# Kernel tuning notes

Hardware: AMD Instinct MI355X
Metric: run time of the kernel (lower is better)

The kernel has to match this reference:

```python
import jax, jax.numpy as jnp
import numpy as np

BRANCH = 16   # children per internal node
DEPTH = 4     # levels 0..4, leaves at level 4
IN = 512
HID = 512

def _level_sizes():
    return [BRANCH ** d for d in range(DEPTH + 1)]

def setup_inputs() -> dict:
    key = jax.random.key(0)
    ks = jax.random.split(key, 9)
    N = sum(_level_sizes())  # 69905
    x = jax.random.normal(ks[0], (N, IN), dtype=jnp.float32)
    s = 1.0 / np.sqrt(IN + HID)  # torch nn.Linear default init bound
    def lin(kw, kb):
        w = jax.random.uniform(kw, (HID, IN + HID), jnp.float32, -s, s)
        b = jax.random.uniform(kb, (HID,), jnp.float32, -s, s)
        return w, b
    wi_w, wi_b = lin(ks[1], ks[2])
    wf_w, wf_b = lin(ks[3], ks[4])
    wo_w, wo_b = lin(ks[5], ks[6])
    wu_w, wu_b = lin(ks[7], ks[8])
    return {"x": x, "wi_w": wi_w, "wi_b": wi_b, "wf_w": wf_w, "wf_b": wf_b,
            "wo_w": wo_w, "wo_b": wo_b, "wu_w": wu_w, "wu_b": wu_b}

def reference(x, wi_w, wi_b, wf_w, wf_b, wo_w, wo_b, wu_w, wu_b):
    sizes = _level_sizes()
    offs = np.concatenate([[0], np.cumsum(sizes)])
    levels = [x[offs[d]:offs[d + 1]] for d in range(DEPTH + 1)]

    def gates(xh):
        i = jax.nn.sigmoid(xh @ wi_w.T + wi_b)
        o = jax.nn.sigmoid(xh @ wo_w.T + wo_b)
        u = jnp.tanh(xh @ wu_w.T + wu_b)
        return i, o, u

    # leaf_forward: h_prev = 0, no forget terms
    Xl = levels[DEPTH]
    xh = jnp.concatenate([Xl, jnp.zeros((Xl.shape[0], HID), Xl.dtype)], axis=1)
    i, o, u = gates(xh)
    C = i * u
    H = o * jnp.tanh(C)

    # node_forward, bottom-up. Faithful quirk of the source: the forget gate
    # is computed on the child CELL state (cat(x, c_k)), not the hidden state.
    for d in range(DEPTH - 1, -1, -1):
        Xd = levels[d]                      # [n, IN]
        n = Xd.shape[0]
        Hc = H.reshape(n, BRANCH, HID)      # children hidden
        Cc = C.reshape(n, BRANCH, HID)      # children cell
        h_sum = Hc.sum(axis=1)
        xh = jnp.concatenate([Xd, h_sum], axis=1)
        i, o, u = gates(xh)
        xc = jnp.concatenate([jnp.broadcast_to(Xd[:, None, :], (n, BRANCH, IN)), Cc], axis=-1)
        f = jax.nn.sigmoid(jnp.einsum('nbk,hk->nbh', xc, wf_w) + wf_b)
        C = i * u + (f * Cc).sum(axis=1)
        H = o * jnp.tanh(C)

    return H[0], C[0]
```

## Files before the change

kernel.cpp:

```cpp
#include <hip/hip_runtime.h>
#include <stdint.h>
#include <stddef.h>


typedef __bf16 bf16x8 __attribute__((ext_vector_type(8)));
typedef float  f32x4  __attribute__((ext_vector_type(4)));
typedef void __attribute__((address_space(3))) lds_void_t;
typedef void __attribute__((address_space(1))) gbl_void_t;

__device__ __forceinline__ uint16_t f2bf(float f) {
  union { float f; uint32_t u; } v; v.f = f;
  return (uint16_t)((v.u + 0x7fffu + ((v.u >> 16) & 1u)) >> 16);
}
__device__ __forceinline__ float bf2f(uint16_t u) {
  union { uint32_t u; float f; } v; v.u = (uint32_t)u << 16;
  return v.f;
}
__device__ __forceinline__ float sig_(float x) {
  return __builtin_amdgcn_rcpf(1.0f + __expf(-x));
}
__device__ __forceinline__ float tanh_(float x) {
  x = fminf(15.f, fmaxf(-15.f, x));
  float e = __expf(2.f * x);
  return (e - 1.f) * __builtin_amdgcn_rcpf(e + 1.f);
}

__global__ void k_conv_x(const float4* __restrict__ src,
                         ushort4* __restrict__ dst, long n4) {
  long i = blockIdx.x * (long)blockDim.x + threadIdx.x;
  long stride = (long)gridDim.x * blockDim.x;
  for (; i < n4; i += stride) {
    float4 v = src[i];
    ushort4 r;
    r.x = f2bf(v.x); r.y = f2bf(v.y); r.z = f2bf(v.z); r.w = f2bf(v.w);
    dst[i] = r;
  }
}
__global__ void k_conv_w(const float4* __restrict__ w0,
                         const float4* __restrict__ w1,
                         const float4* __restrict__ w2,
                         const float4* __restrict__ w3,
                         ushort4* __restrict__ dst) {
  const long per4 = (long)512 * 1024 / 4;
  long i = blockIdx.x * (long)blockDim.x + threadIdx.x;
  long stride = (long)gridDim.x * blockDim.x;
  for (; i < 4 * per4; i += stride) {
    long seg = i / per4, off2 = i - seg * per4;
    const float4* s = (seg == 0) ? w0 : (seg == 1) ? w1 : (seg == 2) ? w2 : w3;
    float4 v = s[off2];
    ushort4 r;
    r.x = f2bf(v.x); r.y = f2bf(v.y); r.z = f2bf(v.z); r.w = f2bf(v.w);
    dst[i] = r;
  }
}

#define BM 128
#define BN 128
#define BK 32

__global__ __launch_bounds__(256)
void k_gemm_bt(const uint16_t* __restrict__ A, int lda,
               const uint16_t* __restrict__ B, int ldb,
               float* __restrict__ C, int ldc, int K) {
  __shared__ uint16_t As[BM * BK];
  __shared__ uint16_t Bs[BN * BK];
  const int tid = threadIdx.x, lane = tid & 63, wave = tid >> 6;
  const int lrow = lane & 15, quad = lane >> 4;
  const int wm = (wave >> 1) * 64, wn = (wave & 1) * 64;
  const long tm = blockIdx.x, tn = blockIdx.y;
  f32x4 acc[4][4] = {};
  const int srow = lane >> 2, scol = (lane & 3) * 8;
  for (int k0 = 0; k0 < K; k0 += BK) {
#pragma unroll
    for (int i = 0; i < 2; ++i) {
      int row = i * 64 + wave * 16 + srow;
      const uint16_t* gp = A + (tm * BM + row) * (long)lda + k0 + scol;
      __builtin_amdgcn_global_load_lds((gbl_void_t*)(uintptr_t)gp,
          (lds_void_t*)&As[i * 2048 + wave * 512], 16, 0, 0);
    }
#pragma unroll
    for (int i = 0; i < 2; ++i) {
      int row = i * 64 + wave * 16 + srow;
      const uint16_t* gp = B + (tn * BN + row) * (long)ldb + k0 + scol;
      __builtin_amdgcn_global_load_lds((gbl_void_t*)(uintptr_t)gp,
          (lds_void_t*)&Bs[i * 2048 + wave * 512], 16, 0, 0);
    }
    __syncthreads();
    bf16x8 a[4], b[4];
#pragma unroll
    for (int f = 0; f < 4; ++f)
      a[f] = *(const bf16x8*)&As[(wm + f * 16 + lrow) * BK + quad * 8];
#pragma unroll
    for (int f = 0; f < 4; ++f)
      b[f] = *(const bf16x8*)&Bs[(wn + f * 16 + lrow) * BK + quad * 8];
#pragma unroll
    for (int fm = 0; fm < 4; ++fm)
#pragma unroll
      for (int fn = 0; fn < 4; ++fn)
        acc[fm][fn] = __builtin_amdgcn_mfma_f32_16x16x32_bf16(
            a[fm], b[fn], acc[fm][fn], 0, 0, 0);
    __syncthreads();
  }
#pragma unroll
  for (int fm = 0; fm < 4; ++fm)
#pragma unroll
    for (int fn = 0; fn < 4; ++fn) {
      long col  = tn * BN + wn + fn * 16 + lrow;
      long row0 = tm * BM + wm + fm * 16 + quad * 4;
#pragma unroll
      for (int r = 0; r < 4; ++r)
        C[(row0 + r) * (long)ldc + col] = acc[fm][fn][r];
    }
}

template <bool HAS_F>
__global__ __launch_bounds__(256, 3)
void k_level(const uint16_t* __restrict__ A, int lda, int K,
             const uint16_t* __restrict__ Wg,
             const float* __restrict__ bi, const float* __restrict__ bo,
             const float* __restrict__ bu,
             const float* __restrict__ Fpart,
             uint16_t* __restrict__ Cbf,
             const uint16_t* __restrict__ Xnext,
             uint16_t* __restrict__ xh_next) {
  __shared__ uint16_t As[2][128 * 32];
  __shared__ uint16_t Bs[2][3 * 64 * 32];
  const int tid = threadIdx.x, lane = tid & 63, wave = tid >> 6;
  const int lrow = lane & 15, quad = lane >> 4;
  const int wm = (wave >> 1) * 64, wn = (wave & 1) * 32;

  long tm, tn;
  {
    const int nTm = (int)(gridDim.x >> 3);
    int b = blockIdx.x;
    if ((nTm & 7) == 0) {
      int x = b & 7, j = b >> 3, per = nTm >> 3;
      tn = j & 7; tm = (long)x * per + (j >> 3);
    } else { tm = b >> 3; tn = b & 7; }
  }

  f32x4 acc[3][4][2] = {};
  const int srow = lane >> 2, scol = (lane & 3) * 8;

  for (int k0 = 0; k0 < K; k0 += 64) {
#pragma unroll
    for (int h = 0; h < 2; ++h) {
      int kk = k0 + h * 32;
#pragma unroll
      for (int i = 0; i < 2; ++i) {
        int row = i * 64 + wave * 16 + srow;
        const uint16_t* gp = A + (tm * 128 + row) * (long)lda + kk + scol;
        __builtin_amdgcn_global_load_lds((gbl_void_t*)(uintptr_t)gp,
            (lds_void_t*)&As[h][i * 2048 + wave * 512], 16, 0, 0);
      }
#pragma unroll
      for (int g = 0; g < 3; ++g) {
        long grow = g * 512 + tn * 64 + wave * 16 + srow;
        const uint16_t* gp = Wg + grow * 1024 + kk + scol;
        __builtin_amdgcn_global_load_lds((gbl_void_t*)(uintptr_t)gp,
            (lds_void_t*)&Bs[h][g * 2048 + wave * 512], 16, 0, 0);
      }
    }
    __syncthreads();

#pragma unroll
    for (int h = 0; h < 2; ++h) {
      bf16x8 a[4];
#pragma unroll
      for (int f = 0; f < 4; ++f)
        a[f] = *(const bf16x8*)&As[h][(wm + f * 16 + lrow) * 32 + quad * 8];
#pragma unroll
      for (int g = 0; g < 3; ++g) {
        bf16x8 b0 = *(const bf16x8*)&Bs[h][g * 2048 + (wn + lrow) * 32 +
                                           quad * 8];
        bf16x8 b1 = *(const bf16x8*)&Bs[h][g * 2048 + (wn + 16 + lrow) * 32 +
                                           quad * 8];
#pragma unroll
        for (int fm = 0; fm < 4; ++fm) {
          acc[g][fm][0] = __builtin_amdgcn_mfma_f32_16x16x32_bf16(
              a[fm], b0, acc[g][fm][0], 0, 0, 0);
          acc[g][fm][1] = __builtin_amdgcn_mfma_f32_16x16x32_bf16(
              a[fm], b1, acc[g][fm][1], 0, 0, 0);
        }
      }
    }
    __syncthreads();
  }

#pragma unroll
  for (int fn = 0; fn < 2; ++fn) {
    long col = tn * 64 + wn + fn * 16 + lrow;
    float biv = bi[col], bov = bo[col], buv = bu[col];
#pragma unroll
    for (int fm = 0; fm < 4; ++fm) {
      long row0 = tm * 128 + wm + fm * 16 + quad * 4;
      long pg   = tm * 8 + (wm >> 4) + fm;
      float hs = 0.f;
#pragma unroll
      for (int r = 0; r < 4; ++r) {
        long row = row0 + r;
        float iv = sig_(acc[0][fm][fn][r] + biv);
        float ov = sig_(acc[1][fm][fn][r] + bov);
        float uv = tanh_(acc[2][fm][fn][r] + buv);
        float c  = iv * uv;
        if (HAS_F) c += Fpart[row * 512 + col];
        Cbf[row * 512 + col] = f2bf(c);
        hs += ov * tanh_(c);
      }
      hs += __shfl_xor(hs, 16, 64);
      hs += __shfl_xor(hs, 32, 64);
      if (quad == 0) {
        xh_next[pg * 1024 + col]       = Xnext[pg * 512 + col];
        xh_next[pg * 1024 + 512 + col] = f2bf(hs);
      }
    }
  }
}

__global__ __launch_bounds__(256, 3)
void k_fc_combine(const uint16_t* __restrict__ Cbf,
                  const uint16_t* __restrict__ Wfc, int ldb,
                  const float* __restrict__ Fx,
                  const float* __restrict__ bfb,
                  float* __restrict__ Fpart) {
  __shared__ uint16_t As[2][BM * BK];
  __shared__ uint16_t Bs[2][BN * BK];
  const int tid = threadIdx.x, lane = tid & 63, wave = tid >> 6;
  const int lrow = lane & 15, quad = lane >> 4;
  const int wm = (wave >> 1) * 64, wn = (wave & 1) * 64;
  long tm, tn;
  {
    const int nTm = (int)(gridDim.x >> 2);
    int b = blockIdx.x;
    if ((nTm & 7) == 0) {
      int x = b & 7, j = b >> 3, per = nTm >> 3;
      tn = j & 3; tm = (long)x * per + (j >> 2);
    } else { tm = b >> 2; tn = b & 3; }
  }
  const int lda = 512;
  f32x4 acc[4][4] = {};
  const int srow = lane >> 2, scol = (lane & 3) * 8;
  for (int k0 = 0; k0 < 512; k0 += 64) {
#pragma unroll
    for (int h = 0; h < 2; ++h) {
      int kk = k0 + h * 32;
#pragma unroll
      for (int i = 0; i < 2; ++i) {
        int row = i * 64 + wave * 16 + srow;
        const uint16_t* gp = Cbf + (tm * BM + row) * (long)lda + kk + scol;
        __builtin_amdgcn_global_load_lds((gbl_void_t*)(uintptr_t)gp,
            (lds_void_t*)&As[h][i * 2048 + wave * 512], 16, 0, 0);
      }
#pragma unroll
      for (int i = 0; i < 2; ++i) {
        int row = i * 64 + wave * 16 + srow;
        const uint16_t* gp = Wfc + (tn * BN + row) * (long)ldb + kk + scol;
        __builtin_amdgcn_global_load_lds((gbl_void_t*)(uintptr_t)gp,
            (lds_void_t*)&Bs[h][i * 2048 + wave * 512], 16, 0, 0);
      }
    }
    __syncthreads();
#pragma unroll
    for (int h = 0; h < 2; ++h) {
      bf16x8 a[4], b[4];
#pragma unroll
      for (int f = 0; f < 4; ++f)
        a[f] = *(const bf16x8*)&As[h][(wm + f * 16 + lrow) * BK + quad * 8];
#pragma unroll
      for (int f = 0; f < 4; ++f)
        b[f] = *(const bf16x8*)&Bs[h][(wn + f * 16 + lrow) * BK + quad * 8];
#pragma unroll
      for (int fm = 0; fm < 4; ++fm)
#pragma unroll
        for (int fn = 0; fn < 4; ++fn)
          acc[fm][fn] = __builtin_amdgcn_mfma_f32_16x16x32_bf16(
              a[fm], b[fn], acc[fm][fn], 0, 0, 0);
    }
    __syncthreads();
  }
#pragma unroll
  for (int fm = 0; fm < 4; ++fm) {
    long pg   = tm * 8 + (wm >> 4) + fm;
    long row0 = tm * BM + wm + fm * 16 + quad * 4;
#pragma unroll
    for (int fn = 0; fn < 4; ++fn) {
      long col = tn * BN + wn + fn * 16 + lrow;
      float fx = Fx[pg * 512 + col] + bfb[col];
      float t = 0.f;
#pragma unroll
      for (int r = 0; r < 4; ++r)
        t += sig_(fx + acc[fm][fn][r]) * bf2f(Cbf[(row0 + r) * 512 + col]);
      t += __shfl_xor(t, 16, 64);
      t += __shfl_xor(t, 32, 64);
      if (quad == 0) Fpart[pg * 512 + col] = t;
    }
  }
}

__global__ void k_dot_bb(const uint16_t* __restrict__ A, int lda,
                         const uint16_t* __restrict__ B, int ldb,
                         float* __restrict__ C, int ldc,
                         int M, int N, int K) {
  int wid  = (int)((blockIdx.x * (long)blockDim.x + threadIdx.x) >> 6);
  int lane = threadIdx.x & 63;
  if (wid >= M * N) return;
  int m = wid / N, n = wid - m * N;
  const uint16_t* a = A + (long)m * lda;
  const uint16_t* b = B + (long)n * ldb;
  int per = K >> 6, k0 = lane * per;
  float s = 0.f;
  for (int j = 0; j < per; j += 4) {
    ushort4 av = *(const ushort4*)(a + k0 + j);
    ushort4 bv = *(const ushort4*)(b + k0 + j);
    s += bf2f(av.x) * bf2f(bv.x) + bf2f(av.y) * bf2f(bv.y)
       + bf2f(av.z) * bf2f(bv.z) + bf2f(av.w) * bf2f(bv.w);
  }
#pragma unroll
  for (int off = 32; off; off >>= 1) s += __shfl_xor(s, off, 64);
  if (lane == 0) C[(long)m * ldc + n] = s;
}
__global__ void k_dot_f32(const float* __restrict__ A, int lda,
                          const float* __restrict__ B, int ldb,
                          float* __restrict__ C, int ldc,
                          int M, int N, int K) {
  int wid  = (int)((blockIdx.x * (long)blockDim.x + threadIdx.x) >> 6);
  int lane = threadIdx.x & 63;
  if (wid >= M * N) return;
  int m = wid / N, n = wid - m * N;
  const float* a = A + (long)m * lda;
  const float* b = B + (long)n * ldb;
  int per = K >> 6, k0 = lane * per;
  float s = 0.f;
  for (int j = 0; j < per; j += 4) {
    float4 av = *(const float4*)(a + k0 + j);
    float4 bv = *(const float4*)(b + k0 + j);
    s += av.x * bv.x + av.y * bv.y + av.z * bv.z + av.w * bv.w;
  }
#pragma unroll
  for (int off = 32; off; off >>= 1) s += __shfl_xor(s, off, 64);
  if (lane == 0) C[(long)m * ldc + n] = s;
}

__global__ void k_hsum_xh4(const float* __restrict__ Hc,
                           const uint16_t* __restrict__ xd,
                           uint16_t* __restrict__ xh, int n) {
  long idx = blockIdx.x * (long)blockDim.x + threadIdx.x;
  if (idx >= (long)n * 128) return;
  long p = idx >> 7; int hq = (int)(idx & 127) << 2;
  const float* hp = Hc + (p << 4) * 512 + hq;
  float4 s = {0.f, 0.f, 0.f, 0.f};
#pragma unroll
  for (int b = 0; b < 16; ++b) {
    float4 v = *(const float4*)(hp + b * 512);
    s.x += v.x; s.y += v.y; s.z += v.z; s.w += v.w;
  }
  *(ushort4*)(xh + p * 1024 + hq) = *(const ushort4*)(xd + p * 512 + hq);
  ushort4 hw = {f2bf(s.x), f2bf(s.y), f2bf(s.z), f2bf(s.w)};
  *(ushort4*)(xh + p * 1024 + 512 + hq) = hw;
}

__global__ void k_combine4(const float* __restrict__ Fc,
                           const float* __restrict__ Fx,
                           const float* __restrict__ bfb,
                           const float* __restrict__ Cc,
                           float* __restrict__ Fpart, int nParents) {
  long idx = blockIdx.x * (long)blockDim.x + threadIdx.x;
  if (idx >= (long)nParents * 128) return;
  long pl = idx >> 7; int hq = (int)(idx & 127) << 2;
  float4 fxv = *(const float4*)(Fx + pl * 512 + hq);
  float4 bfv = *(const float4*)(bfb + hq);
  float fx0 = fxv.x + bfv.x, fx1 = fxv.y + bfv.y;
  float fx2 = fxv.z + bfv.z, fx3 = fxv.w + bfv.w;
  float a0 = 0.f, a1 = 0.f, a2 = 0.f, a3 = 0.f;
#pragma unroll 4
  for (int b = 0; b < 16; ++b) {
    long cl = pl * 16 + b;
    float4 f = *(const float4*)(Fc + cl * 512 + hq);
    float4 c = *(const float4*)(Cc + cl * 512 + hq);
    a0 += sig_(fx0 + f.x) * c.x;
    a1 += sig_(fx1 + f.y) * c.y;
    a2 += sig_(fx2 + f.z) * c.z;
    a3 += sig_(fx3 + f.w) * c.w;
  }
  float4 r = {a0, a1, a2, a3};
  *(float4*)(Fpart + pl * 512 + hq) = r;
}

__global__ void k_final4(const float* __restrict__ G,
                         const float* __restrict__ Fpart,
                         const float* __restrict__ bi,
                         const float* __restrict__ bo,
                         const float* __restrict__ bu,
                         float* __restrict__ H, float* __restrict__ Cv,
                         uint16_t* __restrict__ Cbf, int n) {
  long idx = blockIdx.x * (long)blockDim.x + threadIdx.x;
  if (idx >= (long)n * 128) return;
  long p = idx >> 7; int hq = (int)(idx & 127) << 2;
  const float* g = G + p * 1536;
  float4 gi = *(const float4*)(g + hq);
  float4 go = *(const float4*)(g + 512 + hq);
  float4 gu = *(const float4*)(g + 1024 + hq);
  float4 b_i = *(const float4*)(bi + hq);
  float4 b_o = *(const float4*)(bo + hq);
  float4 b_u = *(const float4*)(bu + hq);
  float4 fp = *(const float4*)(Fpart + p * 512 + hq);
  const float* gip = &gi.x; const float* gop = &go.x; const float* gup = &gu.x;
  const float* bip = &b_i.x; const float* bop = &b_o.x; const float* bup = &b_u.x;
  const float* fpp = &fp.x;
  float4 hv, cv;
  float* hvp = &hv.x; float* cvp = &cv.x;
  ushort4 cw; unsigned short* cwp = &cw.x;
#pragma unroll
  for (int j = 0; j < 4; ++j) {
    float iv = sig_(gip[j] + bip[j]);
    float ov = sig_(gop[j] + bop[j]);
    float uv = tanh_(gup[j] + bup[j]);
    float c  = iv * uv + fpp[j];
    cvp[j] = c;
    cwp[j] = f2bf(c);
    hvp[j] = ov * tanh_(c);
  }
  *(float4*)(H  + p * 512 + hq) = hv;
  *(float4*)(Cv + p * 512 + hq) = cv;
  *(ushort4*)(Cbf + p * 512 + hq) = cw;
}

extern "C" void kernel_launch(void* const* d_in, const int* in_sizes, int n_in,
                              void* d_out, int out_size, void* d_ws, size_t ws_size,
                              hipStream_t stream) {
  const float* x    = (const float*)d_in[0];
  const float* wi_w = (const float*)d_in[1];
  const float* wi_b = (const float*)d_in[2];
  const float* wf_w = (const float*)d_in[3];
  const float* wf_b = (const float*)d_in[4];
  const float* wo_w = (const float*)d_in[5];
  const float* wo_b = (const float*)d_in[6];
  const float* wu_w = (const float*)d_in[7];
  const float* wu_b = (const float*)d_in[8];
  (void)in_sizes; (void)n_in; (void)out_size; (void)ws_size;

  static const long offs[5] = {0, 1, 17, 273, 4369};
  const long NTOT = 69905;

  char* ws = (char*)d_ws;
  size_t off = 0;
  auto alloc = [&](size_t bytes) -> void* {
    void* p = ws + off;
    off += (bytes + 255) & ~(size_t)255;
    return p;
  };
  uint16_t* Xbf   = (uint16_t*)alloc(NTOT * 512 * 2);
  uint16_t* Wgw   = (uint16_t*)alloc((size_t)2048 * 1024 * 2);
  uint16_t* Wg    = Wgw;
  uint16_t* Wf    = Wgw + (size_t)1536 * 1024;
  float*    FxAll = (float*)alloc((size_t)4480 * 512 * 4);
  uint16_t* Cbf   = (uint16_t*)alloc((size_t)65536 * 512 * 2);
  uint16_t* CbfU  = (uint16_t*)alloc((size_t)4096 * 512 * 2);
  uint16_t* CbfU2 = (uint16_t*)alloc((size_t)256 * 512 * 2);
  uint16_t* xhA   = (uint16_t*)alloc((size_t)4096 * 1024 * 2);
  uint16_t* xhB   = (uint16_t*)alloc((size_t)256 * 1024 * 2);
  uint16_t* xhC   = (uint16_t*)alloc((size_t)16 * 1024 * 2);
  float*    Fpart = (float*)alloc((size_t)4096 * 512 * 4);
  float*    Gf    = (float*)alloc((size_t)16 * 1536 * 4);
  float*    Fc    = (float*)alloc((size_t)16 * 512 * 4);
  float*    HupA  = (float*)alloc((size_t)16 * 512 * 4);
  float*    CupA  = (float*)alloc((size_t)16 * 512 * 4);

  auto blks = [](long n) { return (int)((n + 255) / 256); };

  {
    long n4 = NTOT * 512 / 4;
    k_conv_x<<<8192, 256, 0, stream>>>((const float4*)x, (ushort4*)Xbf, n4);
    k_conv_w<<<2048, 256, 0, stream>>>((const float4*)wi_w, (const float4*)wo_w,
                                       (const float4*)wu_w, (const float4*)wf_w,
                                       (ushort4*)Wgw);
  }

  {
    dim3 grid(35, 4);
    k_gemm_bt<<<grid, 256, 0, stream>>>(Xbf, 512, Wf, 1024, FxAll, 512, 512);
  }

  k_level<false><<<4096, 256, 0, stream>>>(
      Xbf + offs[4] * 512, 512, 512, Wg, wi_b, wo_b, wu_b, nullptr,
      Cbf, Xbf + offs[3] * 512, xhA);
  k_fc_combine<<<2048, 256, 0, stream>>>(Cbf, Wf + 512, 1024,
                                         FxAll + offs[3] * 512, wf_b, Fpart);

  k_level<true><<<256, 256, 0, stream>>>(
      xhA, 1024, 1024, Wg, wi_b, wo_b, wu_b, Fpart,
      CbfU, Xbf + offs[2] * 512, xhB);
  k_fc_combine<<<128, 256, 0, stream>>>(CbfU, Wf + 512, 1024,
                                        FxAll + offs[2] * 512, wf_b, Fpart);

  k_level<true><<<16, 256, 0, stream>>>(
      xhB, 1024, 1024, Wg, wi_b, wo_b, wu_b, Fpart,
      CbfU2, Xbf + offs[1] * 512, xhC);
  k_fc_combine<<<8, 256, 0, stream>>>(CbfU2, Wf + 512, 1024,
                                      FxAll + offs[1] * 512, wf_b, Fpart);

  {
    long waves = 16L * 1536;
    k_dot_bb<<<(int)((waves * 64 + 255) / 256), 256, 0, stream>>>(
        xhC, 1024, Wg, 1024, Gf, 1536, 16, 1536, 1024);
    k_final4<<<blks(16L * 128), 256, 0, stream>>>(
        Gf, Fpart, wi_b, wo_b, wu_b, HupA, CupA, CbfU2, 16);
  }

  k_hsum_xh4<<<1, 256, 0, stream>>>(HupA, Xbf + offs[0] * 512, xhC, 1);
  {
    long waves = 1536;
    k_dot_bb<<<(int)((waves * 64 + 255) / 256), 256, 0, stream>>>(
        xhC, 1024, Wg, 1024, Gf, 1536, 1, 1536, 1024);
  }
  {
    long waves = 16L * 512;
    k_dot_f32<<<(int)((waves * 64 + 255) / 256), 256, 0, stream>>>(
        CupA, 512, wf_w + 512, 1024, Fc, 512, 16, 512, 512);
  }
  k_combine4<<<1, 256, 0, stream>>>(Fc, FxAll, wf_b, CupA, Fpart, 1);
  k_final4<<<1, 256, 0, stream>>>(
      Gf, Fpart, wi_b, wo_b, wu_b,
      (float*)d_out, (float*)d_out + 512, CbfU2, 1);
}
```

Measured before the change: 526.4 us.

## Double-buffer LDS tiles in level and fc GEMMs to overlap loads with MFMA

Both GEMM kernels now keep two LDS buffers and issue the global-to-LDS loads for the next K tile before computing the current one. Each stage ends with an explicit vmcnt wait and barrier, and MFMA sections run at raised wave priority. This is meant to hide global load latency that the old load-sync-compute-sync loop exposed. The doubled LDS footprint lowers the occupancy target from 3 to 2 blocks per CU. The change also switches f2bf to the native bf16 conversion and rewrites tanh as 2*sigmoid(2x)-1 to cut ALU work in the epilogues.

```diff
diff --git a/kernel.cpp b/kernel.cpp
--- a/kernel.cpp
+++ b/kernel.cpp
@@ -9,8 +9,9 @@
 typedef void __attribute__((address_space(1))) gbl_void_t;
 
 __device__ __forceinline__ uint16_t f2bf(float f) {
-  union { float f; uint32_t u; } v; v.f = f;
-  return (uint16_t)((v.u + 0x7fffu + ((v.u >> 16) & 1u)) >> 16);
+  union { __bf16 b; uint16_t u; } v;
+  v.b = (__bf16)f;
+  return v.u;
 }
 __device__ __forceinline__ float bf2f(uint16_t u) {
   union { uint32_t u; float f; } v; v.u = (uint32_t)u << 16;
@@ -20,9 +21,8 @@
   return __builtin_amdgcn_rcpf(1.0f + __expf(-x));
 }
 __device__ __forceinline__ float tanh_(float x) {
-  x = fminf(15.f, fmaxf(-15.f, x));
-  float e = __expf(2.f * x);
-  return (e - 1.f) * __builtin_amdgcn_rcpf(e + 1.f);
+  return __builtin_fmaf(2.f,
+      __builtin_amdgcn_rcpf(1.f + __expf(-2.f * x)), -1.f);
 }
 
 __global__ void k_conv_x(const float4* __restrict__ src,
@@ -114,7 +114,7 @@
 }
 
 template <bool HAS_F>
-__global__ __launch_bounds__(256, 3)
+__global__ __launch_bounds__(256, 2)
 void k_level(const uint16_t* __restrict__ A, int lda, int K,
              const uint16_t* __restrict__ Wg,
              const float* __restrict__ bi, const float* __restrict__ bo,
@@ -123,8 +123,8 @@
              uint16_t* __restrict__ Cbf,
              const uint16_t* __restrict__ Xnext,
              uint16_t* __restrict__ xh_next) {
-  __shared__ uint16_t As[2][128 * 32];
-  __shared__ uint16_t Bs[2][3 * 64 * 32];
+  __shared__ uint16_t As[2][2][128 * 32];
+  __shared__ uint16_t Bs[2][2][3 * 64 * 32];
   const int tid = threadIdx.x, lane = tid & 63, wave = tid >> 6;
   const int lrow = lane & 15, quad = lane >> 4;
   const int wm = (wave >> 1) * 64, wn = (wave & 1) * 32;
@@ -142,39 +142,42 @@
   f32x4 acc[3][4][2] = {};
   const int srow = lane >> 2, scol = (lane & 3) * 8;
 
-  for (int k0 = 0; k0 < K; k0 += 64) {
+  auto stage = [&](int kt, int buf) {
 #pragma unroll
     for (int h = 0; h < 2; ++h) {
-      int kk = k0 + h * 32;
+      int kk = kt * 64 + h * 32;
 #pragma unroll
       for (int i = 0; i < 2; ++i) {
         int row = i * 64 + wave * 16 + srow;
         const uint16_t* gp = A + (tm * 128 + row) * (long)lda + kk + scol;
         __builtin_amdgcn_global_load_lds((gbl_void_t*)(uintptr_t)gp,
-            (lds_void_t*)&As[h][i * 2048 + wave * 512], 16, 0, 0);
+            (lds_void_t*)&As[buf][h][i * 2048 + wave * 512], 16, 0, 0);
       }
 #pragma unroll
       for (int g = 0; g < 3; ++g) {
         long grow = g * 512 + tn * 64 + wave * 16 + srow;
         const uint16_t* gp = Wg + grow * 1024 + kk + scol;
         __builtin_amdgcn_global_load_lds((gbl_void_t*)(uintptr_t)gp,
-            (lds_void_t*)&Bs[h][g * 2048 + wave * 512], 16, 0, 0);
-      }
-    }
-    __syncthreads();
-
+            (lds_void_t*)&Bs[buf][h][g * 2048 + wave * 512], 16, 0, 0);
+      }
+    }
+  };
+
+  auto compute = [&](int buf) {
 #pragma unroll
     for (int h = 0; h < 2; ++h) {
       bf16x8 a[4];
 #pragma unroll
       for (int f = 0; f < 4; ++f)
-        a[f] = *(const bf16x8*)&As[h][(wm + f * 16 + lrow) * 32 + quad * 8];
+        a[f] = *(const bf16x8*)&As[buf][h][(wm + f * 16 + lrow) * 32 +
+                                           quad * 8];
 #pragma unroll
       for (int g = 0; g < 3; ++g) {
-        bf16x8 b0 = *(const bf16x8*)&Bs[h][g * 2048 + (wn + lrow) * 32 +
-                                           quad * 8];
-        bf16x8 b1 = *(const bf16x8*)&Bs[h][g * 2048 + (wn + 16 + lrow) * 32 +
-                                           quad * 8];
+        bf16x8 b0 = *(const bf16x8*)&Bs[buf][h][g * 2048 + (wn + lrow) * 32 +
+                                                quad * 8];
+        bf16x8 b1 = *(const bf16x8*)&Bs[buf][h][g * 2048 +
+                                                (wn + 16 + lrow) * 32 +
+                                                quad * 8];
 #pragma unroll
         for (int fm = 0; fm < 4; ++fm) {
           acc[g][fm][0] = __builtin_amdgcn_mfma_f32_16x16x32_bf16(
@@ -184,7 +187,25 @@
         }
       }
     }
-    __syncthreads();
+  };
+
+  const int NT = K >> 6;
+  stage(0, 0);
+  asm volatile("s_waitcnt vmcnt(0)" ::: "memory");
+  __builtin_amdgcn_s_barrier();
+  for (int kt = 0; kt < NT; kt += 2) {
+    stage(kt + 1, 1);
+    __builtin_amdgcn_s_setprio(1);
+    compute(0);
+    __builtin_amdgcn_s_setprio(0);
+    asm volatile("s_waitcnt vmcnt(0)" ::: "memory");
+    __builtin_amdgcn_s_barrier();
+    if (kt + 2 < NT) stage(kt + 2, 0);
+    __builtin_amdgcn_s_setprio(1);
+    compute(1);
+    __builtin_amdgcn_s_setprio(0);
+    asm volatile("s_waitcnt vmcnt(0)" ::: "memory");
+    __builtin_amdgcn_s_barrier();
   }
 
 #pragma unroll
@@ -217,14 +238,14 @@
   }
 }
 
-__global__ __launch_bounds__(256, 3)
+__global__ __launch_bounds__(256, 2)
 void k_fc_combine(const uint16_t* __restrict__ Cbf,
                   const uint16_t* __restrict__ Wfc, int ldb,
                   const float* __restrict__ Fx,
                   const float* __restrict__ bfb,
                   float* __restrict__ Fpart) {
-  __shared__ uint16_t As[2][BM * BK];
-  __shared__ uint16_t Bs[2][BN * BK];
+  __shared__ uint16_t As[2][2][BM * BK];
+  __shared__ uint16_t Bs[2][2][BN * BK];
   const int tid = threadIdx.x, lane = tid & 63, wave = tid >> 6;
   const int lrow = lane & 15, quad = lane >> 4;
   const int wm = (wave >> 1) * 64, wn = (wave & 1) * 64;
@@ -240,35 +261,40 @@
   const int lda = 512;
   f32x4 acc[4][4] = {};
   const int srow = lane >> 2, scol = (lane & 3) * 8;
-  for (int k0 = 0; k0 < 512; k0 += 64) {
+
+  auto stage = [&](int kt, int buf) {
 #pragma unroll
     for (int h = 0; h < 2; ++h) {
-      int kk = k0 + h * 32;
+      int kk = kt * 64 + h * 32;
 #pragma unroll
       for (int i = 0; i < 2; ++i) {
         int row = i * 64 + wave * 16 + srow;
         const uint16_t* gp = Cbf + (tm * BM + row) * (long)lda + kk + scol;
         __builtin_amdgcn_global_load_lds((gbl_void_t*)(uintptr_t)gp,
-            (lds_void_t*)&As[h][i * 2048 + wave * 512], 16, 0, 0);
+            (lds_void_t*)&As[buf][h][i * 2048 + wave * 512], 16, 0, 0);
       }
 #pragma unroll
       for (int i = 0; i < 2; ++i) {
         int row = i * 64 + wave * 16 + srow;
         const uint16_t* gp = Wfc + (tn * BN + row) * (long)ldb + kk + scol;
         __builtin_amdgcn_global_load_lds((gbl_void_t*)(uintptr_t)gp,
-            (lds_void_t*)&Bs[h][i * 2048 + wave * 512], 16, 0, 0);
-      }
-    }
-    __syncthreads();
+            (lds_void_t*)&Bs[buf][h][i * 2048 + wave * 512], 16, 0, 0);
+      }
+    }
+  };
+
+  auto compute = [&](int buf) {
 #pragma unroll
     for (int h = 0; h < 2; ++h) {
       bf16x8 a[4], b[4];
 #pragma unroll
       for (int f = 0; f < 4; ++f)
-        a[f] = *(const bf16x8*)&As[h][(wm + f * 16 + lrow) * BK + quad * 8];
+        a[f] = *(const bf16x8*)&As[buf][h][(wm + f * 16 + lrow) * BK +
+                                           quad * 8];
 #pragma unroll
       for (int f = 0; f < 4; ++f)
-        b[f] = *(const bf16x8*)&Bs[h][(wn + f * 16 + lrow) * BK + quad * 8];
+        b[f] = *(const bf16x8*)&Bs[buf][h][(wn + f * 16 + lrow) * BK +
+                                           quad * 8];
 #pragma unroll
       for (int fm = 0; fm < 4; ++fm)
 #pragma unroll
@@ -276,8 +302,27 @@
           acc[fm][fn] = __builtin_amdgcn_mfma_f32_16x16x32_bf16(
               a[fm], b[fn], acc[fm][fn], 0, 0, 0);
     }
-    __syncthreads();
-  }
+  };
+
+  const int NT = 8;
+  stage(0, 0);
+  asm volatile("s_waitcnt vmcnt(0)" ::: "memory");
+  __builtin_amdgcn_s_barrier();
+  for (int kt = 0; kt < NT; kt += 2) {
+    stage(kt + 1, 1);
+    __builtin_amdgcn_s_setprio(1);
+    compute(0);
+    __builtin_amdgcn_s_setprio(0);
+    asm volatile("s_waitcnt vmcnt(0)" ::: "memory");
+    __builtin_amdgcn_s_barrier();
+    if (kt + 2 < NT) stage(kt + 2, 0);
+    __builtin_amdgcn_s_setprio(1);
+    compute(1);
+    __builtin_amdgcn_s_setprio(0);
+    asm volatile("s_waitcnt vmcnt(0)" ::: "memory");
+    __builtin_amdgcn_s_barrier();
+  }
+
 #pragma unroll
   for (int fm = 0; fm < 4; ++fm) {
     long pg   = tm * 8 + (wm >> 4) + fm;
```

Measured after the change: 553.3 us. 1.05x slower.
